# Kernel optimization log

Measured on AMD Instinct MI355X. Metric: run time of the kernel, lower is better.

## Reference

```python
import jax, jax.numpy as jnp
import numpy as np
import math

D_MODEL = 1024
NUM_HEADS = 16
HEAD_DIM = D_MODEL // NUM_HEADS  # 64
PLANE_DIM = HEAD_DIM // 2        # 32
ROPE_THETA = 10000.0
ROPE_PERIOD = 1024.0
ROPE_SCALE = 2.0 * math.pi / ROPE_PERIOD


def _inv_freq():
    # 1 / theta^(arange(0, plane_dim, 2)/plane_dim)  -> [plane_dim//2] = [16]
    return 1.0 / ROPE_THETA ** (jnp.arange(0, PLANE_DIM, 2, dtype=jnp.float32) / PLANE_DIM)


def _rotate_pairs(x, sin, cos):
    # x: [B,H,N,P], sin/cos: [B,1,N,P//2]
    x0 = x[..., 0::2]
    x1 = x[..., 1::2]
    y0 = x0 * cos - x1 * sin
    y1 = x0 * sin + x1 * cos
    return jnp.stack([y0, y1], axis=-1).reshape(x.shape)


def _apply_rope_2d(x, pos_2d, inv_freq):
    # x: [B,H,N,D], pos_2d: [B,N,2]
    ang_x = pos_2d[..., 0] * ROPE_SCALE  # [B,N]
    ang_y = pos_2d[..., 1] * ROPE_SCALE
    fx = ang_x[..., None] * inv_freq     # [B,N,P//2]
    fy = ang_y[..., None] * inv_freq
    sin_x, cos_x = jnp.sin(fx)[:, None], jnp.cos(fx)[:, None]  # [B,1,N,P//2]
    sin_y, cos_y = jnp.sin(fy)[:, None], jnp.cos(fy)[:, None]
    xp, yp = x[..., :PLANE_DIM], x[..., PLANE_DIM:]
    xp = _rotate_pairs(xp, sin_x, cos_x)
    yp = _rotate_pairs(yp, sin_y, cos_y)
    return jnp.concatenate([xp, yp], axis=-1)


def setup_inputs() -> dict:
    key = jax.random.key(0)
    ks = jax.random.split(key, 12)
    B, N, d = 2, 2048, D_MODEL
    s = 1.0 / math.sqrt(d)
    return {
        "x": jax.random.normal(ks[0], (B, N, d), jnp.float32),
        "q_positions": jax.random.uniform(ks[1], (B, N, 2), jnp.float32) * ROPE_PERIOD,
        "kv_positions": jax.random.uniform(ks[2], (B, N, 2), jnp.float32) * ROPE_PERIOD,
        "Wq": jax.random.normal(ks[3], (d, d), jnp.float32) * s,
        "bq": jnp.zeros((d,), jnp.float32),
        "Wk": jax.random.normal(ks[4], (d, d), jnp.float32) * s,
        "bk": jnp.zeros((d,), jnp.float32),
        "Wv": jax.random.normal(ks[5], (d, d), jnp.float32) * s,
        "bv": jnp.zeros((d,), jnp.float32),
        "Wo": jax.random.normal(ks[6], (d, d), jnp.float32) * s,
        "bo": jnp.zeros((d,), jnp.float32),
    }


def reference(x, q_positions, kv_positions, Wq, bq, Wk, bk, Wv, bv, Wo, bo):
    B, Nq, _ = x.shape
    H, D = NUM_HEADS, HEAD_DIM
    inv_freq = _inv_freq()
    # fused-style QKV projections (torch Linear: x @ W.T + b)
    q = (jnp.einsum('bnd,od->bno', x, Wq) + bq).reshape(B, Nq, H, D).transpose(0, 2, 1, 3)
    k = (jnp.einsum('bnd,od->bno', x, Wk) + bk).reshape(B, Nq, H, D).transpose(0, 2, 1, 3)
    v = (jnp.einsum('bnd,od->bno', x, Wv) + bv).reshape(B, Nq, H, D).transpose(0, 2, 1, 3)
    q = _apply_rope_2d(q, q_positions, inv_freq)
    k = _apply_rope_2d(k, kv_positions, inv_freq)
    logits = jnp.einsum('bhqd,bhkd->bhqk', q, k) / math.sqrt(D)
    attn = jax.nn.softmax(logits, axis=-1)
    out = jnp.einsum('bhqk,bhkd->bhqd', attn, v)
    out = out.transpose(0, 2, 1, 3).reshape(B, Nq, D_MODEL)
    return jnp.einsum('bnd,od->bno', out, Wo) + bo
```

## Files before the change

### kernel.cpp

```cpp
#include <hip/hip_runtime.h>
#include <math.h>

#define SEQ   2048
#define DM    1024
#define NTOK  4096
#define HEADS 16
#define HDIM  64
#define ROPE_SCALE 0.006135923151542565f
#define L2_10000   13.287712379549449f

typedef __attribute__((ext_vector_type(8))) short bf16x8;
typedef __attribute__((ext_vector_type(4))) float f32x4;

__device__ __forceinline__ unsigned short f2bf(float f) {
    unsigned int u = __float_as_uint(f);
    return (unsigned short)((u + 0x7FFFu + ((u >> 16) & 1u)) >> 16);
}
__device__ __forceinline__ float bf2f(unsigned short h) {
    return __uint_as_float(((unsigned int)h) << 16);
}

__device__ __forceinline__ void split8(const float* __restrict__ src, bf16x8& h, bf16x8& l) {
    float4 f0 = ((const float4*)src)[0];
    float4 f1 = ((const float4*)src)[1];
    float fv[8] = {f0.x,f0.y,f0.z,f0.w,f1.x,f1.y,f1.z,f1.w};
    #pragma unroll
    for (int j = 0; j < 8; ++j) {
        unsigned short hb = f2bf(fv[j]);
        h[j] = (short)hb;
        l[j] = (short)f2bf(fv[j] - bf2f(hb));
    }
}

__device__ __forceinline__ void gload16(const void* g, void* l) {
    __builtin_amdgcn_global_load_lds(
        (const __attribute__((address_space(1))) unsigned int*)g,
        (__attribute__((address_space(3))) unsigned int*)l, 16, 0, 0);
}

__global__ __launch_bounds__(256) void pack_swz(
    const float* __restrict__ src, unsigned short* __restrict__ dst)
{
    const int idx = blockIdx.x*256 + threadIdx.x;
    const int e = idx * 8;
    const int r = e >> 10, k0 = e & 1023;
    bf16x8 h, l;
    split8(src + (size_t)r*DM + k0, h, l);
    const int mt = r >> 7, rl = r & 127;
    const int kt = k0 >> 5, kl = k0 & 31;
    char* tb = (char*)(dst + ((size_t)(mt*32 + kt))*8192);
    const int sw = (rl & 7) << 4;
    *(bf16x8*)(tb + ((rl*128 + kl*2) ^ sw))      = h;
    *(bf16x8*)(tb + ((rl*128 + 64 + kl*2) ^ sw)) = l;
}

__global__ __launch_bounds__(256) void pack_swz3(
    const float* __restrict__ Wq, const float* __restrict__ Wk,
    const float* __restrict__ Wv, unsigned short* __restrict__ dst)
{
    const int idx = blockIdx.x*256 + threadIdx.x;
    const int e = idx * 8;
    const int r = e >> 10, k0 = e & 1023;
    const int proj = r >> 10;
    const float* W = proj==0 ? Wq : (proj==1 ? Wk : Wv);
    bf16x8 h, l;
    split8(W + (size_t)(r & 1023)*DM + k0, h, l);
    const int mt = r >> 7, rl = r & 127;
    const int kt = k0 >> 5, kl = k0 & 31;
    char* tb = (char*)(dst + ((size_t)(mt*32 + kt))*8192);
    const int sw = (rl & 7) << 4;
    *(bf16x8*)(tb + ((rl*128 + kl*2) ^ sw))      = h;
    *(bf16x8*)(tb + ((rl*128 + 64 + kl*2) ^ sw)) = l;
}

__global__ __launch_bounds__(256, 3) void gemm_mfma(
    const unsigned short* __restrict__ Ap, const unsigned short* __restrict__ Bp,
    const int mode,
    const float* __restrict__ bq, const float* __restrict__ bk,
    const float* __restrict__ bv,
    const float* __restrict__ qpos, const float* __restrict__ kpos,
    float* __restrict__ qo, float* __restrict__ ko, float* __restrict__ vo,
    const float* __restrict__ bo, float* __restrict__ outp)
{
    __shared__ __align__(16) unsigned short Ab[8192];
    __shared__ __align__(16) unsigned short Bb[8192];

    const int tid = threadIdx.x, lane = tid & 63, wv = tid >> 6;
    const int col = lane & 15, grp = lane >> 4;
    const int wr = wv >> 1, wc = wv & 1;

    const int NX = gridDim.x, NB = NX * gridDim.y;
    const int bid = blockIdx.y * NX + blockIdx.x;
    const int bid2 = (bid & 7) * (NB >> 3) + (bid >> 3);
    const int nt = bid2 % NX, mt = bid2 / NX;

    f32x4 acc[4][4];
    #pragma unroll
    for (int mf=0; mf<4; ++mf)
        #pragma unroll
        for (int nf=0; nf<4; ++nf)
            acc[mf][nf] = (f32x4)0.f;

    for (int kt = 0; kt < 32; ++kt) {
        __syncthreads();
        {
            const char* ga = (const char*)Ap + ((size_t)(mt*32 + kt))*16384;
            const char* gb = (const char*)Bp + ((size_t)(nt*32 + kt))*16384;
            #pragma unroll
            for (int rep = 0; rep < 4; ++rep) {
                const int o = wv*4096 + rep*1024;
                gload16(ga + o + lane*16, (char*)Ab + o);
                gload16(gb + o + lane*16, (char*)Bb + o);
            }
        }
        __syncthreads();
        const char* A = (const char*)Ab;
        const char* B = (const char*)Bb;
        bf16x8 ah[4], al[4];
        #pragma unroll
        for (int mf = 0; mf < 4; ++mf) {
            const int rl = wr*64 + mf*16 + col;
            const int b0 = rl*128 + grp*16;
            const int sw = (rl & 7) << 4;
            ah[mf] = *(const bf16x8*)(A + (b0 ^ sw));
            al[mf] = *(const bf16x8*)(A + ((b0 + 64) ^ sw));
        }
        #pragma unroll
        for (int nf = 0; nf < 4; ++nf) {
            const int rl = wc*64 + nf*16 + col;
            const int b0 = rl*128 + grp*16;
            const int sw = (rl & 7) << 4;
            bf16x8 bh  = *(const bf16x8*)(B + (b0 ^ sw));
            bf16x8 blo = *(const bf16x8*)(B + ((b0 + 64) ^ sw));
            #pragma unroll
            for (int mf = 0; mf < 4; ++mf) {
                acc[mf][nf] = __builtin_amdgcn_mfma_f32_16x16x32_bf16(ah[mf], bh,  acc[mf][nf], 0,0,0);
                acc[mf][nf] = __builtin_amdgcn_mfma_f32_16x16x32_bf16(ah[mf], blo, acc[mf][nf], 0,0,0);
                acc[mf][nf] = __builtin_amdgcn_mfma_f32_16x16x32_bf16(al[mf], bh,  acc[mf][nf], 0,0,0);
            }
        }
    }

    const int m0 = mt*128, n0 = nt*128;
    if (mode == 1) {
        #pragma unroll
        for (int nf = 0; nf < 4; ++nf) {
            const int n = n0 + wc*64 + nf*16 + col;
            const float bn = bo[n];
            #pragma unroll
            for (int mf = 0; mf < 4; ++mf)
                #pragma unroll
                for (int i = 0; i < 4; ++i) {
                    const int tok = m0 + wr*64 + mf*16 + grp*4 + i;
                    outp[(size_t)tok*DM + n] = acc[mf][nf][i] + bn;
                }
        }
    } else {
        const int proj = n0 >> 10;
        const float* bb = proj==0 ? bq : (proj==1 ? bk : bv);
        float* op       = proj==0 ? qo : (proj==1 ? ko : vo);
        const float* pp = proj==0 ? qpos : kpos;
        #pragma unroll
        for (int nf = 0; nf < 4; ++nf) {
            const int n  = n0 + wc*64 + nf*16 + col;
            const int nn = n & 1023;
            const int h  = nn >> 6, dd = nn & 63;
            const float bn = bb[nn];
            if (proj == 2) {
                #pragma unroll
                for (int mf = 0; mf < 4; ++mf)
                    #pragma unroll
                    for (int i = 0; i < 4; ++i) {
                        const int tok = m0 + wr*64 + mf*16 + grp*4 + i;
                        const int b = tok >> 11, sq = tok & 2047;
                        op[(((size_t)(b*HEADS + h))*SEQ + sq)*HDIM + dd] = acc[mf][nf][i] + bn;
                    }
            } else {
                const int plane = dd >> 5;
                const float e = (float)(dd & 30) * (1.0f/32.0f);
                const float invf = exp2f(-L2_10000 * e);
                #pragma unroll
                for (int mf = 0; mf < 4; ++mf)
                    #pragma unroll
                    for (int i = 0; i < 4; ++i) {
                        const int tok = m0 + wr*64 + mf*16 + grp*4 + i;
                        const int b = tok >> 11, sq = tok & 2047;
                        const float pv = pp[((size_t)(b*SEQ + sq))*2 + plane];
                        const float ang = pv * ROPE_SCALE * invf;
                        float s, c;
                        sincosf(ang, &s, &c);
                        const float val = acc[mf][nf][i] + bn;
                        const float prt = __shfl_xor(val, 1);
                        const float res = (dd & 1) ? (prt*s + val*c) : (val*c - prt*s);
                        op[(((size_t)(b*HEADS + h))*SEQ + sq)*HDIM + dd] = res;
                    }
            }
        }
    }
}

#define KB 32

__global__ __launch_bounds__(256) void attn_mfma(
    const float* __restrict__ q, const float* __restrict__ k,
    const float* __restrict__ v, float* __restrict__ ao)
{
    const int bh  = blockIdx.y;
    const int qb0 = blockIdx.x * 128;
    const int tid = threadIdx.x;
    const int lane = tid & 63;
    const int wv   = tid >> 6;
    const int col  = lane & 15;
    const int grp  = lane >> 4;

    __shared__ __align__(16) unsigned short Khi[KB][72];
    __shared__ __align__(16) unsigned short Klo[KB][72];
    __shared__ __align__(16) unsigned short Vthi[HDIM][40];
    __shared__ __align__(16) unsigned short Vtlo[HDIM][40];
    __shared__ __align__(16) unsigned short Pb[4][32][40];

    const float* kbase = k + (size_t)bh*SEQ*HDIM;
    const float* vbase = v + (size_t)bh*SEQ*HDIM;

    bf16x8 qhi[2][2], qlo[2][2];
    #pragma unroll
    for (int mf = 0; mf < 2; ++mf)
        #pragma unroll
        for (int ks = 0; ks < 2; ++ks) {
            const float* p = q + ((size_t)bh*SEQ + qb0 + wv*32 + mf*16 + col)*HDIM
                               + ks*32 + grp*8;
            split8(p, qhi[mf][ks], qlo[mf][ks]);
        }

    f32x4 o[2][4];
    #pragma unroll
    for (int mf=0; mf<2; ++mf)
        #pragma unroll
        for (int nf=0; nf<4; ++nf)
            o[mf][nf] = (f32x4)0.f;
    float mrun[2][4], lrun[2][4];
    #pragma unroll
    for (int mf=0; mf<2; ++mf)
        #pragma unroll
        for (int r=0; r<4; ++r) { mrun[mf][r] = -INFINITY; lrun[mf][r] = 0.f; }

    for (int kt = 0; kt < SEQ; kt += KB) {
        __syncthreads();
        {
            const int row = tid >> 3, c0 = (tid & 7) * 8;
            bf16x8 h, l;
            split8(kbase + (size_t)(kt + row)*HDIM + c0, h, l);
            *(bf16x8*)&Khi[row][c0] = h;
            *(bf16x8*)&Klo[row][c0] = l;
        }
        {
            const int key = tid & 31, db = tid >> 5;
            const float* src = vbase + (size_t)(kt + key)*HDIM + db*8;
            float4 f0 = ((const float4*)src)[0];
            float4 f1 = ((const float4*)src)[1];
            float fv[8] = {f0.x,f0.y,f0.z,f0.w,f1.x,f1.y,f1.z,f1.w};
            #pragma unroll
            for (int j = 0; j < 8; ++j) {
                unsigned short hb = f2bf(fv[j]);
                Vthi[db*8+j][key] = hb;
                Vtlo[db*8+j][key] = f2bf(fv[j] - bf2f(hb));
            }
        }
        __syncthreads();

        f32x4 s[2][2];
        #pragma unroll
        for (int mf=0; mf<2; ++mf)
            #pragma unroll
            for (int nf=0; nf<2; ++nf)
                s[mf][nf] = (f32x4)0.f;
        #pragma unroll
        for (int ks = 0; ks < 2; ++ks) {
            bf16x8 kh[2], kl[2];
            #pragma unroll
            for (int nf = 0; nf < 2; ++nf) {
                kh[nf] = *(const bf16x8*)&Khi[nf*16 + col][ks*32 + grp*8];
                kl[nf] = *(const bf16x8*)&Klo[nf*16 + col][ks*32 + grp*8];
            }
            #pragma unroll
            for (int mf = 0; mf < 2; ++mf)
                #pragma unroll
                for (int nf = 0; nf < 2; ++nf) {
                    s[mf][nf] = __builtin_amdgcn_mfma_f32_16x16x32_bf16(qhi[mf][ks], kh[nf], s[mf][nf], 0,0,0);
                    s[mf][nf] = __builtin_amdgcn_mfma_f32_16x16x32_bf16(qlo[mf][ks], kh[nf], s[mf][nf], 0,0,0);
                    s[mf][nf] = __builtin_amdgcn_mfma_f32_16x16x32_bf16(qhi[mf][ks], kl[nf], s[mf][nf], 0,0,0);
                }
        }

        #pragma unroll
        for (int mf=0; mf<2; ++mf)
            #pragma unroll
            for (int nf=0; nf<2; ++nf)
                s[mf][nf] *= 0.125f;

        #pragma unroll
        for (int mf = 0; mf < 2; ++mf) {
            #pragma unroll
            for (int r = 0; r < 4; ++r) {
                float m2 = fmaxf(s[mf][0][r], s[mf][1][r]);
                m2 = fmaxf(m2, __shfl_xor(m2, 1, 16));
                m2 = fmaxf(m2, __shfl_xor(m2, 2, 16));
                m2 = fmaxf(m2, __shfl_xor(m2, 4, 16));
                m2 = fmaxf(m2, __shfl_xor(m2, 8, 16));
                const float mnew = fmaxf(mrun[mf][r], m2);
                const float corr = __expf(mrun[mf][r] - mnew);
                mrun[mf][r] = mnew;
                const float p0 = __expf(s[mf][0][r] - mnew);
                const float p1 = __expf(s[mf][1][r] - mnew);
                float ts = p0 + p1;
                ts += __shfl_xor(ts, 1, 16);
                ts += __shfl_xor(ts, 2, 16);
                ts += __shfl_xor(ts, 4, 16);
                ts += __shfl_xor(ts, 8, 16);
                lrun[mf][r] = lrun[mf][r]*corr + ts;
                #pragma unroll
                for (int nf=0; nf<4; ++nf) o[mf][nf][r] *= corr;
                Pb[wv][mf*16 + grp*4 + r][col]      = f2bf(p0);
                Pb[wv][mf*16 + grp*4 + r][16 + col] = f2bf(p1);
            }
        }

        bf16x8 pa[2];
        #pragma unroll
        for (int mf=0; mf<2; ++mf)
            pa[mf] = *(const bf16x8*)&Pb[wv][mf*16 + col][grp*8];
        #pragma unroll
        for (int nf = 0; nf < 4; ++nf) {
            bf16x8 vh = *(const bf16x8*)&Vthi[nf*16 + col][grp*8];
            bf16x8 vl = *(const bf16x8*)&Vtlo[nf*16 + col][grp*8];
            #pragma unroll
            for (int mf = 0; mf < 2; ++mf) {
                o[mf][nf] = __builtin_amdgcn_mfma_f32_16x16x32_bf16(pa[mf], vh, o[mf][nf], 0,0,0);
                o[mf][nf] = __builtin_amdgcn_mfma_f32_16x16x32_bf16(pa[mf], vl, o[mf][nf], 0,0,0);
            }
        }
    }

    const int b = bh >> 4, h = bh & 15;
    #pragma unroll
    for (int mf = 0; mf < 2; ++mf)
        #pragma unroll
        for (int r = 0; r < 4; ++r) {
            const float inv = 1.0f / lrun[mf][r];
            const int n = qb0 + wv*32 + mf*16 + grp*4 + r;
            float* orow = ao + (((size_t)b*SEQ + n)*HEADS + h)*HDIM;
            #pragma unroll
            for (int nf = 0; nf < 4; ++nf)
                orow[nf*16 + col] = o[mf][nf][r] * inv;
        }
}

extern "C" void kernel_launch(void* const* d_in, const int* in_sizes, int n_in,
                              void* d_out, int out_size, void* d_ws, size_t ws_size,
                              hipStream_t stream)
{
    const float* x    = (const float*)d_in[0];
    const float* qpos = (const float*)d_in[1];
    const float* kpos = (const float*)d_in[2];
    const float* Wq   = (const float*)d_in[3];
    const float* bq   = (const float*)d_in[4];
    const float* Wk   = (const float*)d_in[5];
    const float* bk   = (const float*)d_in[6];
    const float* Wv   = (const float*)d_in[7];
    const float* bv   = (const float*)d_in[8];
    const float* Wo   = (const float*)d_in[9];
    const float* bo   = (const float*)d_in[10];
    float* out = (float*)d_out;

    float* qw = (float*)d_ws;
    float* kw = qw + (size_t)NTOK*DM;
    float* vw = kw + (size_t)NTOK*DM;
    unsigned short* Xp    = (unsigned short*)(vw + (size_t)NTOK*DM);
    unsigned short* Wqkvp = Xp + (size_t)NTOK*DM*2;
    unsigned short* Wop   = Wqkvp + (size_t)3*DM*DM*2;

    pack_swz <<<2048, 256, 0, stream>>>(x, Xp);
    pack_swz3<<<1536, 256, 0, stream>>>(Wq, Wk, Wv, Wqkvp);
    pack_swz <<< 512, 256, 0, stream>>>(Wo, Wop);

    gemm_mfma<<<dim3(24, 32), 256, 0, stream>>>(
        Xp, Wqkvp, 0, bq, bk, bv, qpos, kpos, qw, kw, vw, nullptr, nullptr);

    attn_mfma<<<dim3(SEQ/128, 2*HEADS), 256, 0, stream>>>(qw, kw, vw, out);

    pack_swz <<<2048, 256, 0, stream>>>(out, Xp);

    gemm_mfma<<<dim3(8, 32), 256, 0, stream>>>(
        Xp, Wop, 1, nullptr, nullptr, nullptr, nullptr, nullptr,
        nullptr, nullptr, nullptr, bo, out);
}
```

Baseline: 671.1 us.

## Fuse fp32-to-bf16 split packing into GEMM tile loads, drop pack kernels

Removes the separate pack_swz and pack_swz3 kernels that converted x, the QKV weights, Wo and the attention output into swizzled hi/lo bf16 tiles. The GEMM now loads fp32 rows directly, splits them into hi/lo bf16 in registers and writes the swizzled layout to LDS. This saves four kernel launches and the extra global write and read of the packed buffers. In exchange the conversion work is repeated for every tile that reuses the same rows, and the async global_load_lds path is replaced by register-staged loads. It also changes the split from round-to-nearest to truncation for the hi part.

Result: no change. 669.7 us (-0.2%).

```diff
diff --git a/kernel.cpp b/kernel.cpp
--- a/kernel.cpp
+++ b/kernel.cpp
@@ -32,49 +32,14 @@
     }
 }
 
-__device__ __forceinline__ void gload16(const void* g, void* l) {
-    __builtin_amdgcn_global_load_lds(
-        (const __attribute__((address_space(1))) unsigned int*)g,
-        (__attribute__((address_space(3))) unsigned int*)l, 16, 0, 0);
-}
-
-__global__ __launch_bounds__(256) void pack_swz(
-    const float* __restrict__ src, unsigned short* __restrict__ dst)
-{
-    const int idx = blockIdx.x*256 + threadIdx.x;
-    const int e = idx * 8;
-    const int r = e >> 10, k0 = e & 1023;
-    bf16x8 h, l;
-    split8(src + (size_t)r*DM + k0, h, l);
-    const int mt = r >> 7, rl = r & 127;
-    const int kt = k0 >> 5, kl = k0 & 31;
-    char* tb = (char*)(dst + ((size_t)(mt*32 + kt))*8192);
-    const int sw = (rl & 7) << 4;
-    *(bf16x8*)(tb + ((rl*128 + kl*2) ^ sw))      = h;
-    *(bf16x8*)(tb + ((rl*128 + 64 + kl*2) ^ sw)) = l;
-}
-
-__global__ __launch_bounds__(256) void pack_swz3(
-    const float* __restrict__ Wq, const float* __restrict__ Wk,
-    const float* __restrict__ Wv, unsigned short* __restrict__ dst)
-{
-    const int idx = blockIdx.x*256 + threadIdx.x;
-    const int e = idx * 8;
-    const int r = e >> 10, k0 = e & 1023;
-    const int proj = r >> 10;
-    const float* W = proj==0 ? Wq : (proj==1 ? Wk : Wv);
-    bf16x8 h, l;
-    split8(W + (size_t)(r & 1023)*DM + k0, h, l);
-    const int mt = r >> 7, rl = r & 127;
-    const int kt = k0 >> 5, kl = k0 & 31;
-    char* tb = (char*)(dst + ((size_t)(mt*32 + kt))*8192);
-    const int sw = (rl & 7) << 4;
-    *(bf16x8*)(tb + ((rl*128 + kl*2) ^ sw))      = h;
-    *(bf16x8*)(tb + ((rl*128 + 64 + kl*2) ^ sw)) = l;
-}
-
-__global__ __launch_bounds__(256, 3) void gemm_mfma(
-    const unsigned short* __restrict__ Ap, const unsigned short* __restrict__ Bp,
+__device__ __forceinline__ unsigned int packtop(unsigned int b0, unsigned int b1) {
+    return (b1 & 0xffff0000u) | (b0 >> 16);
+}
+
+__global__ __launch_bounds__(256, 3) void gemm_fused(
+    const float* __restrict__ A,
+    const float* __restrict__ W0, const float* __restrict__ W1,
+    const float* __restrict__ W2,
     const int mode,
     const float* __restrict__ bq, const float* __restrict__ bk,
     const float* __restrict__ bv,
@@ -94,6 +59,24 @@
     const int bid2 = (bid & 7) * (NB >> 3) + (bid >> 3);
     const int nt = bid2 % NX, mt = bid2 / NX;
 
+    const int proj = (nt * 128) >> 10;
+    const float* Wsel = proj==0 ? W0 : (proj==1 ? W1 : W2);
+
+    const int r  = tid >> 1;
+    const int ch = tid & 1;
+    const float* arow = A    + (size_t)(mt*128 + r)*DM + ch*16;
+    const float* brow = Wsel + (size_t)(((nt*128) & 1023) + r)*DM + ch*16;
+    const int sw   = (r & 7) << 4;
+    const int base = r*128 + ch*32;
+    char* aw_hi1 = (char*)Ab + ((base     ) ^ sw);
+    char* aw_hi2 = (char*)Ab + ((base + 16) ^ sw);
+    char* aw_lo1 = (char*)Ab + ((base + 64) ^ sw);
+    char* aw_lo2 = (char*)Ab + ((base + 80) ^ sw);
+    char* bw_hi1 = (char*)Bb + ((base     ) ^ sw);
+    char* bw_hi2 = (char*)Bb + ((base + 16) ^ sw);
+    char* bw_lo1 = (char*)Bb + ((base + 64) ^ sw);
+    char* bw_lo2 = (char*)Bb + ((base + 80) ^ sw);
+
     f32x4 acc[4][4];
     #pragma unroll
     for (int mf=0; mf<4; ++mf)
@@ -102,36 +85,74 @@
             acc[mf][nf] = (f32x4)0.f;
 
     for (int kt = 0; kt < 32; ++kt) {
+        float4 fa0 = ((const float4*)(arow + kt*32))[0];
+        float4 fa1 = ((const float4*)(arow + kt*32))[1];
+        float4 fa2 = ((const float4*)(arow + kt*32))[2];
+        float4 fa3 = ((const float4*)(arow + kt*32))[3];
+        float4 fb0 = ((const float4*)(brow + kt*32))[0];
+        float4 fb1 = ((const float4*)(brow + kt*32))[1];
+        float4 fb2 = ((const float4*)(brow + kt*32))[2];
+        float4 fb3 = ((const float4*)(brow + kt*32))[3];
+
         __syncthreads();
+
         {
-            const char* ga = (const char*)Ap + ((size_t)(mt*32 + kt))*16384;
-            const char* gb = (const char*)Bp + ((size_t)(nt*32 + kt))*16384;
-            #pragma unroll
-            for (int rep = 0; rep < 4; ++rep) {
-                const int o = wv*4096 + rep*1024;
-                gload16(ga + o + lane*16, (char*)Ab + o);
-                gload16(gb + o + lane*16, (char*)Bb + o);
-            }
-        }
+            const float fe[16] = {fa0.x,fa0.y,fa0.z,fa0.w, fa1.x,fa1.y,fa1.z,fa1.w,
+                                  fa2.x,fa2.y,fa2.z,fa2.w, fa3.x,fa3.y,fa3.z,fa3.w};
+            unsigned int hp[8], lp[8];
+            #pragma unroll
+            for (int i = 0; i < 8; ++i) {
+                const unsigned int b0 = __float_as_uint(fe[2*i]);
+                const unsigned int b1 = __float_as_uint(fe[2*i+1]);
+                hp[i] = packtop(b0, b1);
+                const float l0 = fe[2*i]   - __uint_as_float(b0 & 0xffff0000u);
+                const float l1 = fe[2*i+1] - __uint_as_float(b1 & 0xffff0000u);
+                lp[i] = packtop(__float_as_uint(l0), __float_as_uint(l1));
+            }
+            *(uint4*)aw_hi1 = make_uint4(hp[0],hp[1],hp[2],hp[3]);
+            *(uint4*)aw_hi2 = make_uint4(hp[4],hp[5],hp[6],hp[7]);
+            *(uint4*)aw_lo1 = make_uint4(lp[0],lp[1],lp[2],lp[3]);
+            *(uint4*)aw_lo2 = make_uint4(lp[4],lp[5],lp[6],lp[7]);
+        }
+        {
+            const float fe[16] = {fb0.x,fb0.y,fb0.z,fb0.w, fb1.x,fb1.y,fb1.z,fb1.w,
+                                  fb2.x,fb2.y,fb2.z,fb2.w, fb3.x,fb3.y,fb3.z,fb3.w};
+            unsigned int hp[8], lp[8];
+            #pragma unroll
+            for (int i = 0; i < 8; ++i) {
+                const unsigned int b0 = __float_as_uint(fe[2*i]);
+                const unsigned int b1 = __float_as_uint(fe[2*i+1]);
+                hp[i] = packtop(b0, b1);
+                const float l0 = fe[2*i]   - __uint_as_float(b0 & 0xffff0000u);
+                const float l1 = fe[2*i+1] - __uint_as_float(b1 & 0xffff0000u);
+                lp[i] = packtop(__float_as_uint(l0), __float_as_uint(l1));
+            }
+            *(uint4*)bw_hi1 = make_uint4(hp[0],hp[1],hp[2],hp[3]);
+            *(uint4*)bw_hi2 = make_uint4(hp[4],hp[5],hp[6],hp[7]);
+            *(uint4*)bw_lo1 = make_uint4(lp[0],lp[1],lp[2],lp[3]);
+            *(uint4*)bw_lo2 = make_uint4(lp[4],lp[5],lp[6],lp[7]);
+        }
+
         __syncthreads();
-        const char* A = (const char*)Ab;
-        const char* B = (const char*)Bb;
+
+        const char* Ax = (const char*)Ab;
+        const char* Bx = (const char*)Bb;
         bf16x8 ah[4], al[4];
         #pragma unroll
         for (int mf = 0; mf < 4; ++mf) {
             const int rl = wr*64 + mf*16 + col;
             const int b0 = rl*128 + grp*16;
-            const int sw = (rl & 7) << 4;
-            ah[mf] = *(const bf16x8*)(A + (b0 ^ sw));
-            al[mf] = *(const bf16x8*)(A + ((b0 + 64) ^ sw));
+            const int s2 = (rl & 7) << 4;
+            ah[mf] = *(const bf16x8*)(Ax + (b0 ^ s2));
+            al[mf] = *(const bf16x8*)(Ax + ((b0 + 64) ^ s2));
         }
         #pragma unroll
         for (int nf = 0; nf < 4; ++nf) {
             const int rl = wc*64 + nf*16 + col;
             const int b0 = rl*128 + grp*16;
-            const int sw = (rl & 7) << 4;
-            bf16x8 bh  = *(const bf16x8*)(B + (b0 ^ sw));
-            bf16x8 blo = *(const bf16x8*)(B + ((b0 + 64) ^ sw));
+            const int s2 = (rl & 7) << 4;
+            bf16x8 bh  = *(const bf16x8*)(Bx + (b0 ^ s2));
+            bf16x8 blo = *(const bf16x8*)(Bx + ((b0 + 64) ^ s2));
             #pragma unroll
             for (int mf = 0; mf < 4; ++mf) {
                 acc[mf][nf] = __builtin_amdgcn_mfma_f32_16x16x32_bf16(ah[mf], bh,  acc[mf][nf], 0,0,0);
@@ -156,7 +177,6 @@
                 }
         }
     } else {
-        const int proj = n0 >> 10;
         const float* bb = proj==0 ? bq : (proj==1 ? bk : bv);
         float* op       = proj==0 ? qo : (proj==1 ? ko : vo);
         const float* pp = proj==0 ? qpos : kpos;
@@ -375,22 +395,14 @@
     float* qw = (float*)d_ws;
     float* kw = qw + (size_t)NTOK*DM;
     float* vw = kw + (size_t)NTOK*DM;
-    unsigned short* Xp    = (unsigned short*)(vw + (size_t)NTOK*DM);
-    unsigned short* Wqkvp = Xp + (size_t)NTOK*DM*2;
-    unsigned short* Wop   = Wqkvp + (size_t)3*DM*DM*2;
-
-    pack_swz <<<2048, 256, 0, stream>>>(x, Xp);
-    pack_swz3<<<1536, 256, 0, stream>>>(Wq, Wk, Wv, Wqkvp);
-    pack_swz <<< 512, 256, 0, stream>>>(Wo, Wop);
-
-    gemm_mfma<<<dim3(24, 32), 256, 0, stream>>>(
-        Xp, Wqkvp, 0, bq, bk, bv, qpos, kpos, qw, kw, vw, nullptr, nullptr);
-
-    attn_mfma<<<dim3(SEQ/128, 2*HEADS), 256, 0, stream>>>(qw, kw, vw, out);
-
-    pack_swz <<<2048, 256, 0, stream>>>(out, Xp);
-
-    gemm_mfma<<<dim3(8, 32), 256, 0, stream>>>(
-        Xp, Wop, 1, nullptr, nullptr, nullptr, nullptr, nullptr,
+    float* aw = vw + (size_t)NTOK*DM;
+
+    gemm_fused<<<dim3(24, 32), 256, 0, stream>>>(
+        x, Wq, Wk, Wv, 0, bq, bk, bv, qpos, kpos, qw, kw, vw, nullptr, nullptr);
+
+    attn_mfma<<<dim3(SEQ/128, 2*HEADS), 256, 0, stream>>>(qw, kw, vw, aw);
+
+    gemm_fused<<<dim3(8, 32), 256, 0, stream>>>(
+        aw, Wo, nullptr, nullptr, 1, nullptr, nullptr, nullptr, nullptr, nullptr,
         nullptr, nullptr, nullptr, bo, out);
 }
```

## Emit pre-split bf16 hi/lo Q/K/V from QKV GEMM epilogue, V pre-transposed

Applied to the files above, without the earlier changes.

The QKV projection epilogue now writes Q, K and V already split into bf16 high/low halves instead of fp32, with V stored transposed (head-dim major). The attention kernel loads these directly into registers and shared memory, so it no longer re-splits K/V on every query block or does the scattered transposed V writes into LDS. Global footprint per element is unchanged (two shorts versus one float), but redundant conversion work across the 16 query blocks per head is removed. The workspace is reshuffled and the attention output now goes to a separate buffer. The Q/K epilogue stores become 2-byte scattered writes, which could cost more in the GEMM.

Result: no change. 666.3 us (-0.7%).

```diff
diff --git a/kernel.cpp b/kernel.cpp
--- a/kernel.cpp
+++ b/kernel.cpp
@@ -10,6 +10,7 @@
 #define L2_10000   13.287712379549449f
 
 typedef __attribute__((ext_vector_type(8))) short bf16x8;
+typedef __attribute__((ext_vector_type(4))) unsigned short u16x4;
 typedef __attribute__((ext_vector_type(4))) float f32x4;
 
 __device__ __forceinline__ unsigned short f2bf(float f) {
@@ -79,7 +80,8 @@
     const float* __restrict__ bq, const float* __restrict__ bk,
     const float* __restrict__ bv,
     const float* __restrict__ qpos, const float* __restrict__ kpos,
-    float* __restrict__ qo, float* __restrict__ ko, float* __restrict__ vo,
+    unsigned short* __restrict__ qo, unsigned short* __restrict__ ko,
+    unsigned short* __restrict__ vo,
     const float* __restrict__ bo, float* __restrict__ outp)
 {
     __shared__ __align__(16) unsigned short Ab[8192];
@@ -158,7 +160,7 @@
     } else {
         const int proj = n0 >> 10;
         const float* bb = proj==0 ? bq : (proj==1 ? bk : bv);
-        float* op       = proj==0 ? qo : (proj==1 ? ko : vo);
+        unsigned short* op = proj==0 ? qo : (proj==1 ? ko : vo);
         const float* pp = proj==0 ? qpos : kpos;
         #pragma unroll
         for (int nf = 0; nf < 4; ++nf) {
@@ -168,13 +170,21 @@
             const float bn = bb[nn];
             if (proj == 2) {
                 #pragma unroll
-                for (int mf = 0; mf < 4; ++mf)
+                for (int mf = 0; mf < 4; ++mf) {
+                    const int tok0 = m0 + wr*64 + mf*16 + grp*4;
+                    const int b = tok0 >> 11, sq0 = tok0 & 2047;
+                    u16x4 h4, l4;
                     #pragma unroll
                     for (int i = 0; i < 4; ++i) {
-                        const int tok = m0 + wr*64 + mf*16 + grp*4 + i;
-                        const int b = tok >> 11, sq = tok & 2047;
-                        op[(((size_t)(b*HEADS + h))*SEQ + sq)*HDIM + dd] = acc[mf][nf][i] + bn;
+                        const float val = acc[mf][nf][i] + bn;
+                        unsigned short hb = f2bf(val);
+                        h4[i] = hb;
+                        l4[i] = f2bf(val - bf2f(hb));
                     }
+                    const int bh2 = (b*HEADS + h)*2;
+                    *(u16x4*)(op + ((size_t)(bh2+0)*HDIM + dd)*SEQ + sq0) = h4;
+                    *(u16x4*)(op + ((size_t)(bh2+1)*HDIM + dd)*SEQ + sq0) = l4;
+                }
             } else {
                 const int plane = dd >> 5;
                 const float e = (float)(dd & 30) * (1.0f/32.0f);
@@ -192,7 +202,11 @@
                         const float val = acc[mf][nf][i] + bn;
                         const float prt = __shfl_xor(val, 1);
                         const float res = (dd & 1) ? (prt*s + val*c) : (val*c - prt*s);
-                        op[(((size_t)(b*HEADS + h))*SEQ + sq)*HDIM + dd] = res;
+                        unsigned short hb = f2bf(res);
+                        unsigned short lb = f2bf(res - bf2f(hb));
+                        const int bh2 = (b*HEADS + h)*2;
+                        op[((size_t)(bh2+0)*SEQ + sq)*HDIM + dd] = hb;
+                        op[((size_t)(bh2+1)*SEQ + sq)*HDIM + dd] = lb;
                     }
             }
         }
@@ -202,8 +216,8 @@
 #define KB 32
 
 __global__ __launch_bounds__(256) void attn_mfma(
-    const float* __restrict__ q, const float* __restrict__ k,
-    const float* __restrict__ v, float* __restrict__ ao)
+    const unsigned short* __restrict__ q, const unsigned short* __restrict__ k,
+    const unsigned short* __restrict__ v, float* __restrict__ ao)
 {
     const int bh  = blockIdx.y;
     const int qb0 = blockIdx.x * 128;
@@ -219,18 +233,24 @@
     __shared__ __align__(16) unsigned short Vtlo[HDIM][40];
     __shared__ __align__(16) unsigned short Pb[4][32][40];
 
-    const float* kbase = k + (size_t)bh*SEQ*HDIM;
-    const float* vbase = v + (size_t)bh*SEQ*HDIM;
+    const unsigned short* kh_g = k + (size_t)(bh*2)*SEQ*HDIM;
+    const unsigned short* kl_g = kh_g + (size_t)SEQ*HDIM;
+    const unsigned short* vh_g = v + (size_t)(bh*2)*HDIM*SEQ;
+    const unsigned short* vl_g = vh_g + (size_t)HDIM*SEQ;
 
     bf16x8 qhi[2][2], qlo[2][2];
-    #pragma unroll
-    for (int mf = 0; mf < 2; ++mf)
-        #pragma unroll
-        for (int ks = 0; ks < 2; ++ks) {
-            const float* p = q + ((size_t)bh*SEQ + qb0 + wv*32 + mf*16 + col)*HDIM
-                               + ks*32 + grp*8;
-            split8(p, qhi[mf][ks], qlo[mf][ks]);
-        }
+    {
+        const unsigned short* qh_g = q + (size_t)(bh*2)*SEQ*HDIM;
+        const unsigned short* ql_g = qh_g + (size_t)SEQ*HDIM;
+        #pragma unroll
+        for (int mf = 0; mf < 2; ++mf)
+            #pragma unroll
+            for (int ks = 0; ks < 2; ++ks) {
+                const size_t off = (size_t)(qb0 + wv*32 + mf*16 + col)*HDIM + ks*32 + grp*8;
+                qhi[mf][ks] = *(const bf16x8*)(qh_g + off);
+                qlo[mf][ks] = *(const bf16x8*)(ql_g + off);
+            }
+    }
 
     f32x4 o[2][4];
     #pragma unroll
@@ -248,23 +268,15 @@
         __syncthreads();
         {
             const int row = tid >> 3, c0 = (tid & 7) * 8;
-            bf16x8 h, l;
-            split8(kbase + (size_t)(kt + row)*HDIM + c0, h, l);
-            *(bf16x8*)&Khi[row][c0] = h;
-            *(bf16x8*)&Klo[row][c0] = l;
+            const size_t off = (size_t)(kt + row)*HDIM + c0;
+            *(bf16x8*)&Khi[row][c0] = *(const bf16x8*)(kh_g + off);
+            *(bf16x8*)&Klo[row][c0] = *(const bf16x8*)(kl_g + off);
         }
         {
-            const int key = tid & 31, db = tid >> 5;
-            const float* src = vbase + (size_t)(kt + key)*HDIM + db*8;
-            float4 f0 = ((const float4*)src)[0];
-            float4 f1 = ((const float4*)src)[1];
-            float fv[8] = {f0.x,f0.y,f0.z,f0.w,f1.x,f1.y,f1.z,f1.w};
-            #pragma unroll
-            for (int j = 0; j < 8; ++j) {
-                unsigned short hb = f2bf(fv[j]);
-                Vthi[db*8+j][key] = hb;
-                Vtlo[db*8+j][key] = f2bf(fv[j] - bf2f(hb));
-            }
+            const int d = tid >> 2, c = (tid & 3) * 8;
+            const size_t off = (size_t)d*SEQ + kt + c;
+            *(bf16x8*)&Vthi[d][c] = *(const bf16x8*)(vh_g + off);
+            *(bf16x8*)&Vtlo[d][c] = *(const bf16x8*)(vl_g + off);
         }
         __syncthreads();
 
@@ -372,25 +384,27 @@
     const float* bo   = (const float*)d_in[10];
     float* out = (float*)d_out;
 
-    float* qw = (float*)d_ws;
-    float* kw = qw + (size_t)NTOK*DM;
-    float* vw = kw + (size_t)NTOK*DM;
-    unsigned short* Xp    = (unsigned short*)(vw + (size_t)NTOK*DM);
-    unsigned short* Wqkvp = Xp + (size_t)NTOK*DM*2;
-    unsigned short* Wop   = Wqkvp + (size_t)3*DM*DM*2;
+    unsigned short* qp = (unsigned short*)d_ws;
+    unsigned short* kp = qp + (size_t)8388608;
+    unsigned short* vp = kp + (size_t)8388608;
+    unsigned short* Xp = vp + (size_t)8388608;
+    float*          aw = (float*)Xp;
+    unsigned short* Wqkvp = Xp + (size_t)8388608;
+    unsigned short* Wop   = Wqkvp + (size_t)6291456;
+    unsigned short* Ap2   = qp;
 
     pack_swz <<<2048, 256, 0, stream>>>(x, Xp);
     pack_swz3<<<1536, 256, 0, stream>>>(Wq, Wk, Wv, Wqkvp);
     pack_swz <<< 512, 256, 0, stream>>>(Wo, Wop);
 
     gemm_mfma<<<dim3(24, 32), 256, 0, stream>>>(
-        Xp, Wqkvp, 0, bq, bk, bv, qpos, kpos, qw, kw, vw, nullptr, nullptr);
-
-    attn_mfma<<<dim3(SEQ/128, 2*HEADS), 256, 0, stream>>>(qw, kw, vw, out);
-
-    pack_swz <<<2048, 256, 0, stream>>>(out, Xp);
+        Xp, Wqkvp, 0, bq, bk, bv, qpos, kpos, qp, kp, vp, nullptr, nullptr);
+
+    attn_mfma<<<dim3(SEQ/128, 2*HEADS), 256, 0, stream>>>(qp, kp, vp, aw);
+
+    pack_swz <<<2048, 256, 0, stream>>>(aw, Ap2);
 
     gemm_mfma<<<dim3(8, 32), 256, 0, stream>>>(
-        Xp, Wop, 1, nullptr, nullptr, nullptr, nullptr, nullptr,
+        Ap2, Wop, 1, nullptr, nullptr, nullptr, nullptr, nullptr,
         nullptr, nullptr, nullptr, bo, out);
 }
```
